# Performance work log

Measured on AMD Instinct MI355X. Metric: run time of the kernel, lower is better.

## Reference

```python
import jax, jax.numpy as jnp
import numpy as np

N_NODES = 100000
HID = 128
N_LAYERS = 3
N_EDGES = 1600000
EPS = 1e-5


def setup_inputs() -> dict:
    key = jax.random.key(0)
    ks = jax.random.split(key, 10)
    H, L = HID, N_LAYERS
    # edge_index: row 0 = src, row 1 = dst (PyG source_to_target flow)
    edge_index = jax.random.randint(ks[0], (2, N_EDGES), 0, N_NODES, dtype=jnp.int32)
    # xavier-uniform embedding
    lim = float(np.sqrt(6.0 / (N_NODES + H)))
    emb = jax.random.uniform(ks[1], (N_NODES, H), jnp.float32, -lim, lim)
    s = 1.0 / np.sqrt(H)
    Wl = jax.random.uniform(ks[2], (L, H, H), jnp.float32, -s, s)  # lin_l (neighbors), has bias
    bl = jax.random.uniform(ks[3], (L, H), jnp.float32, -s, s)
    Wr = jax.random.uniform(ks[4], (L, H, H), jnp.float32, -s, s)  # lin_r (root), no bias
    ln_gamma = jnp.ones((L, H), jnp.float32)
    ln_beta = jnp.zeros((L, H), jnp.float32)
    sj = 1.0 / np.sqrt(H * (L + 1))
    jkW = jax.random.uniform(ks[5], (H, H * (L + 1)), jnp.float32, -sj, sj)
    jkb = jax.random.uniform(ks[6], (H,), jnp.float32, -sj, sj)
    return {"emb": emb, "Wl": Wl, "bl": bl, "Wr": Wr,
            "ln_gamma": ln_gamma, "ln_beta": ln_beta,
            "jkW": jkW, "jkb": jkb, "edge_index": edge_index}


def _layernorm(x, gamma, beta):
    mu = jnp.mean(x, axis=-1, keepdims=True)
    var = jnp.mean(jnp.square(x - mu), axis=-1, keepdims=True)
    return (x - mu) * jax.lax.rsqrt(var + EPS) * gamma + beta


def reference(emb, Wl, bl, Wr, ln_gamma, ln_beta, jkW, jkb, edge_index):
    src, dst = edge_index[0], edge_index[1]
    n = emb.shape[0]
    # in-degree for mean aggregation (clamped to avoid div-by-zero)
    deg = jax.ops.segment_sum(jnp.ones_like(dst, dtype=emb.dtype), dst, num_segments=n)
    inv_deg = (1.0 / jnp.maximum(deg, 1.0))[:, None]
    x = emb
    xs = [x]
    for i in range(N_LAYERS):
        x_prev = x
        # scatter-mean of neighbor features (gather [E,H] -> segment_sum [N,H])
        agg = jax.ops.segment_sum(x[src], dst, num_segments=n) * inv_deg
        # SAGEConv: lin_l(agg) + lin_r(x)
        x = agg @ Wl[i].T + bl[i] + x @ Wr[i].T
        x = _layernorm(x, ln_gamma[i], ln_beta[i])
        x = jax.nn.relu(x)
        # dropout is identity in eval mode
        if i > 0:
            x = x + x_prev
        xs.append(x)
    # jumping-knowledge concat + projection
    x = jnp.concatenate(xs, axis=1) @ jkW.T + jkb
    return x
```

## Files before the change

kernel.cpp:

```cpp
#include <hip/hip_runtime.h>
#include <hip/hip_bf16.h>
#include <stdint.h>

#define HID 128
#define BSHIFT 7
#define NBLK 64

typedef __attribute__((ext_vector_type(8))) __bf16 bf16x8;
typedef __attribute__((ext_vector_type(4))) float f32x4;
typedef __attribute__((ext_vector_type(2))) float f32x2;

static __device__ __forceinline__ float bf2f(ushort h){
  union { uint u; float f; } c; c.u = ((uint)h) << 16; return c.f;
}
static __device__ __forceinline__ float u2f(uint u){
  union { uint u; float f; } c; c.u = u; return c.f;
}
static __device__ __forceinline__ ushort f2bf(float f){
  union { float f; uint u; } c; c.f = f;
  uint u = c.u;
  return (ushort)((u + 0x7fffu + ((u >> 16) & 1u)) >> 16);
}
static __device__ __forceinline__ bf16x8 load8(const ushort* p){
  return *(const bf16x8*)p;
}

__global__ void k_cvt(const float* __restrict__ in, ushort* __restrict__ out, int n){
  int i = blockIdx.x * 256 + threadIdx.x;
  if (i < n) out[i] = f2bf(in[i]);
}

__global__ void k_cvtw(const float* __restrict__ Wl, const float* __restrict__ Wr,
                       ushort* __restrict__ outF, int total){
  int o = blockIdx.x * 256 + threadIdx.x;
  if (o >= total) return;
  int layer = o >> 15;
  int r = o & 32767;
  int e    = r & 7;
  int lane = (r >> 3) & 63;
  int jt   = (r >> 9) & 7;
  int mat  = (r >> 12) & 1;
  int kt   = r >> 13;
  int l16 = lane & 15, quad = lane >> 4;
  int j = l16 * 8 + jt;
  int k = kt * 32 + quad * 8 + e;
  const float* W = mat ? Wr : Wl;
  outF[o] = f2bf(W[layer * 16384 + j * 128 + k]);
}

__global__ void k_cvtjk(const float* __restrict__ jkW, ushort* __restrict__ outF){
  int o = blockIdx.x * 256 + threadIdx.x;
  int e    = o & 7;
  int lane = (o >> 3) & 63;
  int jt   = (o >> 9) & 7;
  int kt   = o >> 12;
  int l16 = lane & 15, quad = lane >> 4;
  int j = l16 * 4 + (jt & 3) + (jt >> 2) * 64;
  int k = kt * 32 + quad * 8 + e;
  outF[o] = f2bf(jkW[j * 512 + k]);
}

__global__ __launch_bounds__(1024) void k_count(
    const int* __restrict__ dst, int* __restrict__ rowcnt, int E, int NB, int es){
  __shared__ int h[1024];
  int blk = blockIdx.x;
  for (int i = threadIdx.x; i < NB; i += 1024) h[i] = 0;
  __syncthreads();
  int e0 = blk * es, e1 = min(e0 + es, E);
  for (int e = e0 + threadIdx.x; e < e1; e += 1024)
    atomicAdd(&h[dst[e] >> BSHIFT], 1);
  __syncthreads();
  for (int i = threadIdx.x; i < NB; i += 1024)
    rowcnt[blk * NB + i] = h[i];
}

__global__ __launch_bounds__(1024) void k_colscan(
    int* __restrict__ rowcnt, int* __restrict__ bbase, int NB, int nblk){
  int b = threadIdx.x;
  int total = 0;
  if (b < NB)
    for (int r = 0; r < nblk; r++) total += rowcnt[r * NB + b];
  int lane = b & 63, w = b >> 6;
  int x = total;
  #pragma unroll
  for (int d = 1; d < 64; d <<= 1){ int y = __shfl_up(x, d, 64); if (lane >= d) x += y; }
  __shared__ int tmp[16];
  if (lane == 63) tmp[w] = x;
  __syncthreads();
  if (b < 64){
    int s = (lane < 16) ? tmp[lane] : 0;
    #pragma unroll
    for (int d = 1; d < 16; d <<= 1){ int y = __shfl_up(s, d, 64); if (lane >= d) s += y; }
    if (lane < 16) tmp[lane] = s;
  }
  __syncthreads();
  int base = ((w > 0) ? tmp[w - 1] : 0) + x - total;
  if (b < NB){
    bbase[b] = base;
    int acc = base;
    for (int r = 0; r < nblk; r++){
      int v = rowcnt[r * NB + b];
      rowcnt[r * NB + b] = acc;
      acc += v;
    }
    if (b == NB - 1) bbase[NB] = acc;
  }
}

__global__ __launch_bounds__(1024) void k_place(
    const int* __restrict__ src, const int* __restrict__ dst,
    const int* __restrict__ rowcnt, uint* __restrict__ binned, int E, int NB, int es){
  __shared__ int cur[1024];
  int blk = blockIdx.x;
  for (int i = threadIdx.x; i < NB; i += 1024) cur[i] = rowcnt[blk * NB + i];
  __syncthreads();
  int e0 = blk * es, e1 = min(e0 + es, E);
  for (int e = e0 + threadIdx.x; e < e1; e += 1024){
    int d = dst[e];
    int b = d >> BSHIFT;
    int pos = atomicAdd(&cur[b], 1);
    binned[pos] = ((uint)src[e] << BSHIFT) | (uint)(d & 127);
  }
}

__global__ __launch_bounds__(256) void k_bpass(
    const uint* __restrict__ binned, const int* __restrict__ bbase,
    int* __restrict__ csr, int* __restrict__ offs, int* __restrict__ cnt, int N){
  int b = blockIdx.x;
  int n0 = b << BSHIFT;
  int tid = threadIdx.x;
  __shared__ int lcnt[128], loffs[128];
  if (tid < 128) lcnt[tid] = 0;
  __syncthreads();
  int base = bbase[b];
  int m = bbase[b + 1] - base;
  const uint* bp = binned + base;
  uint vv[12]; int slot[12];
  #pragma unroll
  for (int u = 0; u < 12; u++){
    int i = tid + u * 256;
    if (i < m){
      uint v = bp[i];
      vv[u] = v;
      slot[u] = atomicAdd(&lcnt[v & 127], 1);
    }
  }
  __syncthreads();
  if (tid < 64){
    int a0 = lcnt[tid * 2], a1 = lcnt[tid * 2 + 1];
    int s = a0 + a1;
    int x = s;
    #pragma unroll
    for (int d = 1; d < 64; d <<= 1){ int y = __shfl_up(x, d, 64); if (tid >= d) x += y; }
    int excl = x - s;
    loffs[tid * 2] = excl;
    loffs[tid * 2 + 1] = excl + a0;
  }
  __syncthreads();
  if (tid < 128 && n0 + tid < N){
    cnt[n0 + tid] = lcnt[tid];
    offs[n0 + tid] = base + loffs[tid];
  }
  #pragma unroll
  for (int u = 0; u < 12; u++){
    int i = tid + u * 256;
    if (i < m){
      uint v = vv[u];
      csr[base + loffs[v & 127] + slot[u]] = (int)(v >> BSHIFT);
    }
  }
}

__global__ __launch_bounds__(256) void k_aggregate(
    const ushort* __restrict__ x, const int* __restrict__ csr,
    const int* __restrict__ offs, const int* __restrict__ cnt,
    ushort* __restrict__ agg, int N){
  int node = blockIdx.x * 4 + (threadIdx.x >> 6);
  int lane = threadIdx.x & 63;
  if (node >= N) return;
  int grp = lane >> 4;
  int l16 = lane & 15;
  uint lb  = (uint)(l16 << 4);
  int beg = offs[node], d = cnt[node];
  if (d == 0){
    if (grp == 0){
      uint4 z = {0u, 0u, 0u, 0u};
      *(uint4*)(agg + (size_t)node * HID + l16 * 8) = z;
    }
    return;
  }
  const int* __restrict__ cp = csr + beg;
  const char* __restrict__ xb = (const char*)x;
  f32x2 s0 = {0.f,0.f}, s1 = {0.f,0.f}, s2 = {0.f,0.f}, s3 = {0.f,0.f};
  int i = 0;
  for (; i + 8 <= d; i += 8){
    uint o0 = ((uint)cp[i + grp] << 8) + lb;
    uint o1 = ((uint)cp[i + 4 + grp] << 8) + lb;
    uint4 v0 = *(const uint4*)(xb + o0);
    uint4 v1 = *(const uint4*)(xb + o1);
    f32x2 t;
    t.x = u2f(v0.x << 16); t.y = u2f(v0.x & 0xffff0000u); s0 += t;
    t.x = u2f(v0.y << 16); t.y = u2f(v0.y & 0xffff0000u); s1 += t;
    t.x = u2f(v0.z << 16); t.y = u2f(v0.z & 0xffff0000u); s2 += t;
    t.x = u2f(v0.w << 16); t.y = u2f(v0.w & 0xffff0000u); s3 += t;
    t.x = u2f(v1.x << 16); t.y = u2f(v1.x & 0xffff0000u); s0 += t;
    t.x = u2f(v1.y << 16); t.y = u2f(v1.y & 0xffff0000u); s1 += t;
    t.x = u2f(v1.z << 16); t.y = u2f(v1.z & 0xffff0000u); s2 += t;
    t.x = u2f(v1.w << 16); t.y = u2f(v1.w & 0xffff0000u); s3 += t;
  }
  if (i < d){
    int p0 = i + grp, p1 = i + 4 + grp;
    bool k0 = p0 < d, k1 = p1 < d;
    uint o0 = ((uint)cp[k0 ? p0 : d - 1] << 8) + lb;
    uint o1 = ((uint)cp[k1 ? p1 : d - 1] << 8) + lb;
    uint4 v0 = *(const uint4*)(xb + o0);
    uint4 v1 = *(const uint4*)(xb + o1);
    uint ax, ay, az, aw;
    ax = k0 ? v0.x : 0u; ay = k0 ? v0.y : 0u; az = k0 ? v0.z : 0u; aw = k0 ? v0.w : 0u;
    f32x2 t;
    t.x = u2f(ax << 16); t.y = u2f(ax & 0xffff0000u); s0 += t;
    t.x = u2f(ay << 16); t.y = u2f(ay & 0xffff0000u); s1 += t;
    t.x = u2f(az << 16); t.y = u2f(az & 0xffff0000u); s2 += t;
    t.x = u2f(aw << 16); t.y = u2f(aw & 0xffff0000u); s3 += t;
    ax = k1 ? v1.x : 0u; ay = k1 ? v1.y : 0u; az = k1 ? v1.z : 0u; aw = k1 ? v1.w : 0u;
    t.x = u2f(ax << 16); t.y = u2f(ax & 0xffff0000u); s0 += t;
    t.x = u2f(ay << 16); t.y = u2f(ay & 0xffff0000u); s1 += t;
    t.x = u2f(az << 16); t.y = u2f(az & 0xffff0000u); s2 += t;
    t.x = u2f(aw << 16); t.y = u2f(aw & 0xffff0000u); s3 += t;
  }
  #pragma unroll
  for (int m = 16; m < 64; m <<= 1){
    s0.x += __shfl_xor(s0.x, m, 64); s0.y += __shfl_xor(s0.y, m, 64);
    s1.x += __shfl_xor(s1.x, m, 64); s1.y += __shfl_xor(s1.y, m, 64);
    s2.x += __shfl_xor(s2.x, m, 64); s2.y += __shfl_xor(s2.y, m, 64);
    s3.x += __shfl_xor(s3.x, m, 64); s3.y += __shfl_xor(s3.y, m, 64);
  }
  if (grp == 0){
    float inv = 1.0f / fmaxf((float)d, 1.0f);
    uint4 o;
    o.x = (uint)f2bf(s0.x * inv) | ((uint)f2bf(s0.y * inv) << 16);
    o.y = (uint)f2bf(s1.x * inv) | ((uint)f2bf(s1.y * inv) << 16);
    o.z = (uint)f2bf(s2.x * inv) | ((uint)f2bf(s2.y * inv) << 16);
    o.w = (uint)f2bf(s3.x * inv) | ((uint)f2bf(s3.y * inv) << 16);
    *(uint4*)(agg + (size_t)node * HID + l16 * 8) = o;
  }
}

template<int HAS_RES>
__global__ __launch_bounds__(256, 4) void k_layer(
    const ushort* __restrict__ agg, const ushort* __restrict__ xin,
    const ushort* __restrict__ Wf,
    const float* __restrict__ bl, const float* __restrict__ gamma,
    const float* __restrict__ beta,
    ushort* __restrict__ xout, int N){
  int tid = threadIdx.x;
  int wv = tid >> 6, lane = tid & 63;
  int quad = lane >> 4, l16 = lane & 15;
  int rowbase = blockIdx.x * 128 + wv * 32;
  int r0 = rowbase + l16;      if (r0 >= N) r0 = N - 1;
  int r1 = rowbase + 16 + l16; if (r1 >= N) r1 = N - 1;
  int aq = quad * 8;

  const ushort* pa0 = agg + (size_t)r0 * HID;
  const ushort* pa1 = agg + (size_t)r1 * HID;
  const ushort* px0 = xin + (size_t)r0 * HID;
  const ushort* px1 = xin + (size_t)r1 * HID;

  f32x4 acc[2][8];
  {
    float4 bi0 = *(const float4*)(bl + l16 * 8);
    float4 bi1 = *(const float4*)(bl + l16 * 8 + 4);
    float bia[8] = {bi0.x, bi0.y, bi0.z, bi0.w, bi1.x, bi1.y, bi1.z, bi1.w};
    #pragma unroll
    for (int jt = 0; jt < 8; jt++){
      float b = bia[jt];
      f32x4 c = {b, b, b, b};
      acc[0][jt] = c; acc[1][jt] = c;
    }
  }

  bf16x8 c0 = load8(pa0 + aq), c1 = load8(pa1 + aq);
  bf16x8 c2 = load8(px0 + aq), c3 = load8(px1 + aq);
  #pragma unroll
  for (int kt = 0; kt < 4; kt++){
    bf16x8 n0 = c0, n1 = c1, n2 = c2, n3 = c3;
    if (kt < 3){
      int ao = (kt + 1) * 32 + aq;
      n0 = load8(pa0 + ao); n1 = load8(pa1 + ao);
      n2 = load8(px0 + ao); n3 = load8(px1 + ao);
    }
    #pragma unroll
    for (int jt = 0; jt < 8; jt++){
      bf16x8 bL = load8(Wf + ((kt * 16 + jt) * 64 + lane) * 8);
      bf16x8 bR = load8(Wf + ((kt * 16 + 8 + jt) * 64 + lane) * 8);
      acc[0][jt] = __builtin_amdgcn_mfma_f32_16x16x32_bf16(c0, bL, acc[0][jt], 0, 0, 0);
      acc[1][jt] = __builtin_amdgcn_mfma_f32_16x16x32_bf16(c1, bL, acc[1][jt], 0, 0, 0);
      acc[0][jt] = __builtin_amdgcn_mfma_f32_16x16x32_bf16(c2, bR, acc[0][jt], 0, 0, 0);
      acc[1][jt] = __builtin_amdgcn_mfma_f32_16x16x32_bf16(c3, bR, acc[1][jt], 0, 0, 0);
    }
    c0 = n0; c1 = n1; c2 = n2; c3 = n3;
  }

  float4 g0 = *(const float4*)(gamma + l16 * 8);
  float4 g1 = *(const float4*)(gamma + l16 * 8 + 4);
  float4 be0 = *(const float4*)(beta + l16 * 8);
  float4 be1 = *(const float4*)(beta + l16 * 8 + 4);
  float gg[8] = {g0.x, g0.y, g0.z, g0.w, g1.x, g1.y, g1.z, g1.w};
  float bb[8] = {be0.x, be0.y, be0.z, be0.w, be1.x, be1.y, be1.z, be1.w};

  #pragma unroll
  for (int rt = 0; rt < 2; rt++){
    float s1[4] = {0,0,0,0}, s2[4] = {0,0,0,0};
    #pragma unroll
    for (int jt = 0; jt < 8; jt++){
      #pragma unroll
      for (int r = 0; r < 4; r++){ float v = acc[rt][jt][r]; s1[r] += v; s2[r] += v * v; }
    }
    #pragma unroll
    for (int m = 1; m < 16; m <<= 1){
      #pragma unroll
      for (int r = 0; r < 4; r++){
        s1[r] += __shfl_xor(s1[r], m, 64);
        s2[r] += __shfl_xor(s2[r], m, 64);
      }
    }
    #pragma unroll
    for (int r = 0; r < 4; r++){
      float mu = s1[r] * (1.f / 128.f);
      float var = s2[r] * (1.f / 128.f) - mu * mu;
      float rs = rsqrtf(var + 1e-5f);
      int row = rowbase + rt * 16 + quad * 4 + r;
      int rowc = row < N ? row : N - 1;
      uint rw[4] = {0u, 0u, 0u, 0u};
      if (HAS_RES){
        uint4 rv = *(const uint4*)(xin + (size_t)rowc * HID + l16 * 8);
        rw[0] = rv.x; rw[1] = rv.y; rw[2] = rv.z; rw[3] = rv.w;
      }
      uint ow[4];
      #pragma unroll
      for (int p = 0; p < 4; p++){
        float v0 = (acc[rt][2 * p][r] - mu) * rs * gg[2 * p] + bb[2 * p];
        float v1 = (acc[rt][2 * p + 1][r] - mu) * rs * gg[2 * p + 1] + bb[2 * p + 1];
        v0 = fmaxf(v0, 0.f);
        v1 = fmaxf(v1, 0.f);
        if (HAS_RES){
          v0 += bf2f((ushort)(rw[p] & 0xffffu));
          v1 += bf2f((ushort)(rw[p] >> 16));
        }
        ow[p] = (uint)f2bf(v0) | ((uint)f2bf(v1) << 16);
      }
      uint4 o;
      o.x = ow[0]; o.y = ow[1]; o.z = ow[2]; o.w = ow[3];
      if (row < N)
        *(uint4*)(xout + (size_t)row * HID + l16 * 8) = o;
    }
  }
}

__global__ __launch_bounds__(256, 4) void k_jk(
    const ushort* __restrict__ emb, const ushort* __restrict__ x1,
    const ushort* __restrict__ x2, const ushort* __restrict__ x3,
    const ushort* __restrict__ Wf,
    const float* __restrict__ jkb, float* __restrict__ out, int N){
  int tid = threadIdx.x;
  int wv = tid >> 6, lane = tid & 63;
  int quad = lane >> 4, l16 = lane & 15;
  int rowbase = blockIdx.x * 128 + wv * 32;
  int r0 = rowbase + l16;      if (r0 >= N) r0 = N - 1;
  int r1 = rowbase + 16 + l16; if (r1 >= N) r1 = N - 1;
  int aq = quad * 8;
  size_t o0 = (size_t)r0 * HID, o1 = (size_t)r1 * HID;

  f32x4 acc[2][8];
  #pragma unroll
  for (int jt = 0; jt < 8; jt++){
    f32x4 z = {0.f, 0.f, 0.f, 0.f};
    acc[0][jt] = z; acc[1][jt] = z;
  }

  const ushort* srcs[4] = {emb, x1, x2, x3};
  bf16x8 a0 = load8(emb + o0 + aq);
  bf16x8 a1 = load8(emb + o1 + aq);
  #pragma unroll
  for (int ktg = 0; ktg < 16; ktg++){
    bf16x8 n0 = a0, n1 = a1;
    if (ktg < 15){
      const ushort* sp = srcs[(ktg + 1) >> 2];
      int ao = ((ktg + 1) & 3) * 32 + aq;
      n0 = load8(sp + o0 + ao);
      n1 = load8(sp + o1 + ao);
    }
    #pragma unroll
    for (int jt = 0; jt < 8; jt++){
      bf16x8 bW = load8(Wf + ((ktg * 8 + jt) * 64 + lane) * 8);
      acc[0][jt] = __builtin_amdgcn_mfma_f32_16x16x32_bf16(a0, bW, acc[0][jt], 0, 0, 0);
      acc[1][jt] = __builtin_amdgcn_mfma_f32_16x16x32_bf16(a1, bW, acc[1][jt], 0, 0, 0);
    }
    a0 = n0; a1 = n1;
  }

  float4 jb0 = *(const float4*)(jkb + l16 * 4);
  float4 jb1 = *(const float4*)(jkb + 64 + l16 * 4);
  float bia[8] = {jb0.x, jb0.y, jb0.z, jb0.w, jb1.x, jb1.y, jb1.z, jb1.w};

  #pragma unroll
  for (int rt = 0; rt < 2; rt++){
    #pragma unroll
    for (int r = 0; r < 4; r++){
      int row = rowbase + rt * 16 + quad * 4 + r;
      if (row < N){
        f32x4 v0 = {acc[rt][0][r] + bia[0], acc[rt][1][r] + bia[1],
                    acc[rt][2][r] + bia[2], acc[rt][3][r] + bia[3]};
        f32x4 v1 = {acc[rt][4][r] + bia[4], acc[rt][5][r] + bia[5],
                    acc[rt][6][r] + bia[6], acc[rt][7][r] + bia[7]};
        *(f32x4*)(out + (size_t)row * HID + l16 * 4) = v0;
        *(f32x4*)(out + (size_t)row * HID + 64 + l16 * 4) = v1;
      }
    }
  }
}

extern "C" void kernel_launch(void* const* d_in, const int* in_sizes, int n_in,
                              void* d_out, int out_size, void* d_ws, size_t ws_size,
                              hipStream_t stream){
  const float* emb   = (const float*)d_in[0];
  const float* Wl    = (const float*)d_in[1];
  const float* bl    = (const float*)d_in[2];
  const float* Wr    = (const float*)d_in[3];
  const float* gamma = (const float*)d_in[4];
  const float* beta  = (const float*)d_in[5];
  const float* jkW   = (const float*)d_in[6];
  const float* jkb   = (const float*)d_in[7];
  const int*   eidx  = (const int*)d_in[8];
  int N = in_sizes[0] / HID;
  int E = in_sizes[8] / 2;
  const int* src = eidx;
  const int* dst = eidx + E;
  float* out = (float*)d_out;

  int NB = (N + 127) >> BSHIFT;
  int es = (E + NBLK - 1) / NBLK;

  char* w = (char*)d_ws;
  auto carve = [&](size_t bytes) -> char* {
    char* p = w; w += (bytes + 255) & ~(size_t)255; return p;
  };
  int Npad = ((N + 127) / 128) * 128;
  int* rowcnt   = (int*)carve((size_t)NBLK * NB * 4);
  int* bbase    = (int*)carve((size_t)(NB + 1) * 4);
  uint* binned  = (uint*)carve((size_t)E * 4);
  int* cnt      = (int*)carve((size_t)N * 4);
  int* offs     = (int*)carve((size_t)N * 4);
  int* csr      = (int*)carve((size_t)E * 4);
  ushort* Wfrag = (ushort*)carve((size_t)3 * 32768 * 2);
  ushort* jkWf  = (ushort*)carve((size_t)65536 * 2);
  ushort* embbf = (ushort*)carve((size_t)Npad * HID * 2);
  ushort* agg   = (ushort*)carve((size_t)Npad * HID * 2);
  ushort* x1    = (ushort*)carve((size_t)Npad * HID * 2);
  ushort* x2    = (ushort*)carve((size_t)Npad * HID * 2);
  ushort* x3    = (ushort*)carve((size_t)Npad * HID * 2);

  int nEmb = N * HID;
  k_cvtw<<<(3 * 32768 + 255) / 256, 256, 0, stream>>>(Wl, Wr, Wfrag, 3 * 32768);
  k_cvtjk<<<65536 / 256, 256, 0, stream>>>(jkW, jkWf);
  k_cvt<<<(nEmb + 255) / 256, 256, 0, stream>>>(emb, embbf, nEmb);

  k_count<<<NBLK, 1024, 0, stream>>>(dst, rowcnt, E, NB, es);
  k_colscan<<<1, 1024, 0, stream>>>(rowcnt, bbase, NB, NBLK);
  k_place<<<NBLK, 1024, 0, stream>>>(src, dst, rowcnt, binned, E, NB, es);
  k_bpass<<<NB, 256, 0, stream>>>(binned, bbase, csr, offs, cnt, N);

  int aggBlocks = (N + 3) / 4;
  int gemmBlocks = (N + 127) / 128;

  k_aggregate<<<aggBlocks, 256, 0, stream>>>(embbf, csr, offs, cnt, agg, N);
  k_layer<0><<<gemmBlocks, 256, 0, stream>>>(agg, embbf, Wfrag, bl, gamma, beta, x1, N);
  k_aggregate<<<aggBlocks, 256, 0, stream>>>(x1, csr, offs, cnt, agg, N);
  k_layer<1><<<gemmBlocks, 256, 0, stream>>>(agg, x1, Wfrag + 32768, bl + HID,
                                             gamma + HID, beta + HID, x2, N);
  k_aggregate<<<aggBlocks, 256, 0, stream>>>(x2, csr, offs, cnt, agg, N);
  k_layer<1><<<gemmBlocks, 256, 0, stream>>>(agg, x2, Wfrag + 2 * 32768, bl + 2 * HID,
                                             gamma + 2 * HID, beta + 2 * HID, x3, N);
  k_jk<<<gemmBlocks, 256, 0, stream>>>(embbf, x1, x2, x3, jkWf, jkb, out, N);
}
```

Measured before the change: 522.5 us.

## Fuse final SAGE layer with jumping-knowledge projection via shared-memory handoff

The third layer's GEMM, LayerNorm, ReLU and residual are merged into the JK projection kernel. The layer-3 output tile stays in swizzled LDS and feeds the last K-chunk of the JK GEMM, so x3 is never written to or read back from global memory and one launch is removed. The cost is a 32KB LDS allocation per block and higher register pressure from two accumulator sets, which may lower occupancy.

```diff
diff --git a/kernel.cpp b/kernel.cpp
--- a/kernel.cpp
+++ b/kernel.cpp
@@ -357,11 +357,15 @@
   }
 }
 
-__global__ __launch_bounds__(256, 4) void k_jk(
+__global__ __launch_bounds__(256, 4) void k_layerjk(
+    const ushort* __restrict__ agg, const ushort* __restrict__ xin,
     const ushort* __restrict__ emb, const ushort* __restrict__ x1,
-    const ushort* __restrict__ x2, const ushort* __restrict__ x3,
     const ushort* __restrict__ Wf,
-    const float* __restrict__ jkb, float* __restrict__ out, int N){
+    const ushort* __restrict__ Wjk,
+    const float* __restrict__ bl, const float* __restrict__ gamma,
+    const float* __restrict__ beta, const float* __restrict__ jkb,
+    float* __restrict__ out, int N){
+  __shared__ ushort sX[16384];
   int tid = threadIdx.x;
   int wv = tid >> 6, lane = tid & 63;
   int quad = lane >> 4, l16 = lane & 15;
@@ -369,22 +373,114 @@
   int r0 = rowbase + l16;      if (r0 >= N) r0 = N - 1;
   int r1 = rowbase + 16 + l16; if (r1 >= N) r1 = N - 1;
   int aq = quad * 8;
-  size_t o0 = (size_t)r0 * HID, o1 = (size_t)r1 * HID;
+  char* __restrict__ sXb = (char*)sX;
+
+  const ushort* pa0 = agg + (size_t)r0 * HID;
+  const ushort* pa1 = agg + (size_t)r1 * HID;
+  const ushort* px0 = xin + (size_t)r0 * HID;
+  const ushort* px1 = xin + (size_t)r1 * HID;
 
   f32x4 acc[2][8];
+  {
+    float4 bi0 = *(const float4*)(bl + l16 * 8);
+    float4 bi1 = *(const float4*)(bl + l16 * 8 + 4);
+    float bia[8] = {bi0.x, bi0.y, bi0.z, bi0.w, bi1.x, bi1.y, bi1.z, bi1.w};
+    #pragma unroll
+    for (int jt = 0; jt < 8; jt++){
+      float b = bia[jt];
+      f32x4 c = {b, b, b, b};
+      acc[0][jt] = c; acc[1][jt] = c;
+    }
+  }
+
+  bf16x8 c0 = load8(pa0 + aq), c1 = load8(pa1 + aq);
+  bf16x8 c2 = load8(px0 + aq), c3 = load8(px1 + aq);
+  #pragma unroll
+  for (int kt = 0; kt < 4; kt++){
+    bf16x8 n0 = c0, n1 = c1, n2 = c2, n3 = c3;
+    if (kt < 3){
+      int ao = (kt + 1) * 32 + aq;
+      n0 = load8(pa0 + ao); n1 = load8(pa1 + ao);
+      n2 = load8(px0 + ao); n3 = load8(px1 + ao);
+    }
+    #pragma unroll
+    for (int jt = 0; jt < 8; jt++){
+      bf16x8 bL = load8(Wf + ((kt * 16 + jt) * 64 + lane) * 8);
+      bf16x8 bR = load8(Wf + ((kt * 16 + 8 + jt) * 64 + lane) * 8);
+      acc[0][jt] = __builtin_amdgcn_mfma_f32_16x16x32_bf16(c0, bL, acc[0][jt], 0, 0, 0);
+      acc[1][jt] = __builtin_amdgcn_mfma_f32_16x16x32_bf16(c1, bL, acc[1][jt], 0, 0, 0);
+      acc[0][jt] = __builtin_amdgcn_mfma_f32_16x16x32_bf16(c2, bR, acc[0][jt], 0, 0, 0);
+      acc[1][jt] = __builtin_amdgcn_mfma_f32_16x16x32_bf16(c3, bR, acc[1][jt], 0, 0, 0);
+    }
+    c0 = n0; c1 = n1; c2 = n2; c3 = n3;
+  }
+
+  {
+    float4 g0 = *(const float4*)(gamma + l16 * 8);
+    float4 g1 = *(const float4*)(gamma + l16 * 8 + 4);
+    float4 be0 = *(const float4*)(beta + l16 * 8);
+    float4 be1 = *(const float4*)(beta + l16 * 8 + 4);
+    float gg[8] = {g0.x, g0.y, g0.z, g0.w, g1.x, g1.y, g1.z, g1.w};
+    float bb[8] = {be0.x, be0.y, be0.z, be0.w, be1.x, be1.y, be1.z, be1.w};
+
+    #pragma unroll
+    for (int rt = 0; rt < 2; rt++){
+      float s1[4] = {0,0,0,0}, s2[4] = {0,0,0,0};
+      #pragma unroll
+      for (int jt = 0; jt < 8; jt++){
+        #pragma unroll
+        for (int r = 0; r < 4; r++){ float v = acc[rt][jt][r]; s1[r] += v; s2[r] += v * v; }
+      }
+      #pragma unroll
+      for (int m = 1; m < 16; m <<= 1){
+        #pragma unroll
+        for (int r = 0; r < 4; r++){
+          s1[r] += __shfl_xor(s1[r], m, 64);
+          s2[r] += __shfl_xor(s2[r], m, 64);
+        }
+      }
+      #pragma unroll
+      for (int r = 0; r < 4; r++){
+        float mu = s1[r] * (1.f / 128.f);
+        float var = s2[r] * (1.f / 128.f) - mu * mu;
+        float rs = rsqrtf(var + 1e-5f);
+        int row = rowbase + rt * 16 + quad * 4 + r;
+        int rowc = row < N ? row : N - 1;
+        uint4 rv = *(const uint4*)(xin + (size_t)rowc * HID + l16 * 8);
+        uint rw[4] = {rv.x, rv.y, rv.z, rv.w};
+        uint ow[4];
+        #pragma unroll
+        for (int p = 0; p < 4; p++){
+          float v0 = (acc[rt][2 * p][r] - mu) * rs * gg[2 * p] + bb[2 * p];
+          float v1 = (acc[rt][2 * p + 1][r] - mu) * rs * gg[2 * p + 1] + bb[2 * p + 1];
+          v0 = fmaxf(v0, 0.f) + bf2f((ushort)(rw[p] & 0xffffu));
+          v1 = fmaxf(v1, 0.f) + bf2f((ushort)(rw[p] >> 16));
+          ow[p] = (uint)f2bf(v0) | ((uint)f2bf(v1) << 16);
+        }
+        uint4 o;
+        o.x = ow[0]; o.y = ow[1]; o.z = ow[2]; o.w = ow[3];
+        uint lrow = (uint)(wv * 32 + rt * 16 + quad * 4 + r);
+        uint wo = (lrow << 8) + ((uint)(l16 * 16) ^ ((lrow & 7) << 4));
+        *(uint4*)(sXb + wo) = o;
+      }
+    }
+  }
+
+  f32x4 accj[2][8];
   #pragma unroll
   for (int jt = 0; jt < 8; jt++){
     f32x4 z = {0.f, 0.f, 0.f, 0.f};
-    acc[0][jt] = z; acc[1][jt] = z;
-  }
-
-  const ushort* srcs[4] = {emb, x1, x2, x3};
+    accj[0][jt] = z; accj[1][jt] = z;
+  }
+
+  size_t o0 = (size_t)r0 * HID, o1 = (size_t)r1 * HID;
+  const ushort* srcs[3] = {emb, x1, xin};
   bf16x8 a0 = load8(emb + o0 + aq);
   bf16x8 a1 = load8(emb + o1 + aq);
   #pragma unroll
-  for (int ktg = 0; ktg < 16; ktg++){
+  for (int ktg = 0; ktg < 12; ktg++){
     bf16x8 n0 = a0, n1 = a1;
-    if (ktg < 15){
+    if (ktg < 11){
       const ushort* sp = srcs[(ktg + 1) >> 2];
       int ao = ((ktg + 1) & 3) * 32 + aq;
       n0 = load8(sp + o0 + ao);
@@ -392,11 +488,27 @@
     }
     #pragma unroll
     for (int jt = 0; jt < 8; jt++){
-      bf16x8 bW = load8(Wf + ((ktg * 8 + jt) * 64 + lane) * 8);
-      acc[0][jt] = __builtin_amdgcn_mfma_f32_16x16x32_bf16(a0, bW, acc[0][jt], 0, 0, 0);
-      acc[1][jt] = __builtin_amdgcn_mfma_f32_16x16x32_bf16(a1, bW, acc[1][jt], 0, 0, 0);
+      bf16x8 bW = load8(Wjk + ((ktg * 8 + jt) * 64 + lane) * 8);
+      accj[0][jt] = __builtin_amdgcn_mfma_f32_16x16x32_bf16(a0, bW, accj[0][jt], 0, 0, 0);
+      accj[1][jt] = __builtin_amdgcn_mfma_f32_16x16x32_bf16(a1, bW, accj[1][jt], 0, 0, 0);
     }
     a0 = n0; a1 = n1;
+  }
+  {
+    int lr0 = wv * 32 + l16, lr1 = lr0 + 16;
+    #pragma unroll
+    for (int kt = 0; kt < 4; kt++){
+      uint bo = (uint)(kt * 64 + quad * 16);
+      bf16x8 aL0 = *(const bf16x8*)(sXb + ((uint)lr0 << 8) + (bo ^ ((uint)(lr0 & 7) << 4)));
+      bf16x8 aL1 = *(const bf16x8*)(sXb + ((uint)lr1 << 8) + (bo ^ ((uint)(lr1 & 7) << 4)));
+      int ktg = 12 + kt;
+      #pragma unroll
+      for (int jt = 0; jt < 8; jt++){
+        bf16x8 bW = load8(Wjk + ((ktg * 8 + jt) * 64 + lane) * 8);
+        accj[0][jt] = __builtin_amdgcn_mfma_f32_16x16x32_bf16(aL0, bW, accj[0][jt], 0, 0, 0);
+        accj[1][jt] = __builtin_amdgcn_mfma_f32_16x16x32_bf16(aL1, bW, accj[1][jt], 0, 0, 0);
+      }
+    }
   }
 
   float4 jb0 = *(const float4*)(jkb + l16 * 4);
@@ -409,10 +521,10 @@
     for (int r = 0; r < 4; r++){
       int row = rowbase + rt * 16 + quad * 4 + r;
       if (row < N){
-        f32x4 v0 = {acc[rt][0][r] + bia[0], acc[rt][1][r] + bia[1],
-                    acc[rt][2][r] + bia[2], acc[rt][3][r] + bia[3]};
-        f32x4 v1 = {acc[rt][4][r] + bia[4], acc[rt][5][r] + bia[5],
-                    acc[rt][6][r] + bia[6], acc[rt][7][r] + bia[7]};
+        f32x4 v0 = {accj[rt][0][r] + bia[0], accj[rt][1][r] + bia[1],
+                    accj[rt][2][r] + bia[2], accj[rt][3][r] + bia[3]};
+        f32x4 v1 = {accj[rt][4][r] + bia[4], accj[rt][5][r] + bia[5],
+                    accj[rt][6][r] + bia[6], accj[rt][7][r] + bia[7]};
         *(f32x4*)(out + (size_t)row * HID + l16 * 4) = v0;
         *(f32x4*)(out + (size_t)row * HID + 64 + l16 * 4) = v1;
       }
@@ -458,7 +570,6 @@
   ushort* agg   = (ushort*)carve((size_t)Npad * HID * 2);
   ushort* x1    = (ushort*)carve((size_t)Npad * HID * 2);
   ushort* x2    = (ushort*)carve((size_t)Npad * HID * 2);
-  ushort* x3    = (ushort*)carve((size_t)Npad * HID * 2);
 
   int nEmb = N * HID;
   k_cvtw<<<(3 * 32768 + 255) / 256, 256, 0, stream>>>(Wl, Wr, Wfrag, 3 * 32768);
@@ -479,7 +590,7 @@
   k_layer<1><<<gemmBlocks, 256, 0, stream>>>(agg, x1, Wfrag + 32768, bl + HID,
                                              gamma + HID, beta + HID, x2, N);
   k_aggregate<<<aggBlocks, 256, 0, stream>>>(x2, csr, offs, cnt, agg, N);
-  k_layer<1><<<gemmBlocks, 256, 0, stream>>>(agg, x2, Wfrag + 2 * 32768, bl + 2 * HID,
-                                             gamma + 2 * HID, beta + 2 * HID, x3, N);
-  k_jk<<<gemmBlocks, 256, 0, stream>>>(embbf, x1, x2, x3, jkWf, jkb, out, N);
-}
+  k_layerjk<<<gemmBlocks, 256, 0, stream>>>(agg, x2, embbf, x1,
+      Wfrag + 2 * 32768, jkWf, bl + 2 * HID, gamma + 2 * HID, beta + 2 * HID,
+      jkb, out, N);
+}
```

After: 562.2 us. +7.6%, slower.
